# Optimization experiments

Hardware: AMD Instinct MI355X
Metric: run time of the kernel (lower is better)

Reference implementation:

```python
import jax, jax.numpy as jnp
import numpy as np

B, S, D = 64, 1024, 128
EPS = 1e-5

def hardswish(x):
    return x * jnp.clip(x + 3.0, 0.0, 6.0) / 6.0

def setup_inputs() -> dict:
    key = jax.random.key(0)
    k1, k2, k3 = jax.random.split(key, 3)
    x = jax.random.normal(k1, (B, S, D), dtype=jnp.float32)
    ln_w = jnp.ones((S, D), dtype=jnp.float32)
    ln_b = jnp.zeros((S, D), dtype=jnp.float32)
    # U1[i]/U2[i] rows packed into lower-triangular (S,S); init ~ N(0,1)*0.01
    W1 = jax.random.normal(k2, (S, S), dtype=jnp.float32) * 0.01
    W2 = jax.random.normal(k3, (S, S), dtype=jnp.float32) * 0.01
    return {"x": x, "ln_w": ln_w, "ln_b": ln_b, "W1": W1, "W2": W2}

def reference(x, ln_w, ln_b, W1, W2):
    # LayerNorm over the last two dims (seq_len, feature_dim) jointly
    mu = jnp.mean(x, axis=(-2, -1), keepdims=True)
    var = jnp.mean(jnp.square(x - mu), axis=(-2, -1), keepdims=True)
    h = (x - mu) * jax.lax.rsqrt(var + EPS) * ln_w + ln_b
    # causal (lower-triangular) time mixing: u[:, t] = sum_{s<=t} W1[t, s] * h[:, s]
    mask = jnp.tril(jnp.ones((S, S), dtype=x.dtype))
    u = hardswish(jnp.einsum('ts,bsd->btd', W1 * mask, h))
    v = jnp.einsum('ts,bsd->btd', W2 * mask, u)
    return x + v
```

## Files before the change

kernel.cpp:

```cpp
#include <hip/hip_runtime.h>
#include <hip/hip_bf16.h>

#define NB 64
#define S_ 1024
#define D_ 128

typedef __attribute__((ext_vector_type(8))) short bf16x8;
typedef __attribute__((ext_vector_type(4))) float f32x4;

__device__ __forceinline__ unsigned short f2bf(float f) {
  __hip_bfloat16 h = __float2bfloat16(f);
  return __builtin_bit_cast(unsigned short, h);
}

__device__ __forceinline__ void async_copy16(const void* g, void* l) {
  __builtin_amdgcn_global_load_lds(
      (const __attribute__((address_space(1))) unsigned int*)g,
      (__attribute__((address_space(3))) unsigned int*)l, 16, 0, 0);
}

__global__ __launch_bounds__(256) void prep_kernel(
    const float* __restrict__ x, const float* __restrict__ W1,
    const float* __restrict__ W2, float2* __restrict__ part,
    unsigned short* __restrict__ W1b, unsigned short* __restrict__ W2b) {
  const int blk = blockIdx.x;
  if (blk < 1024) {
    const int b = blk >> 4, c = blk & 15, t = threadIdx.x;
    const float4* xb = (const float4*)(x + (size_t)b * (S_ * D_) + c * 8192);
    float s = 0.f, q = 0.f;
#pragma unroll
    for (int i = 0; i < 8; ++i) {
      float4 v = xb[i * 256 + t];
      s += v.x + v.y + v.z + v.w;
      q += v.x * v.x + v.y * v.y + v.z * v.z + v.w * v.w;
    }
#pragma unroll
    for (int o = 32; o > 0; o >>= 1) {
      s += __shfl_down(s, o, 64);
      q += __shfl_down(q, o, 64);
    }
    __shared__ float2 w4[4];
    const int wave = t >> 6, lane = t & 63;
    if (lane == 0) w4[wave] = make_float2(s, q);
    __syncthreads();
    if (t == 0) {
      float ss = 0.f, qq = 0.f;
#pragma unroll
      for (int i = 0; i < 4; ++i) { ss += w4[i].x; qq += w4[i].y; }
      part[blk] = make_float2(ss, qq);
    }
  } else {
    const int id = (blk - 1024) * 256 + threadIdx.x;
    const int perW = (S_ * S_) / 4;
    const float* src = (id < perW) ? W1 : W2;
    unsigned short* dst = (id < perW) ? W1b : W2b;
    const int i4 = (id < perW) ? id : id - perW;
    const int flat = i4 * 4;
    const int trow = flat >> 10;
    const int scol = flat & 1023;
    float4 v = ((const float4*)src)[i4];
    ushort4 o;
    o.x = f2bf((scol + 0 <= trow) ? v.x : 0.f);
    o.y = f2bf((scol + 1 <= trow) ? v.y : 0.f);
    o.z = f2bf((scol + 2 <= trow) ? v.z : 0.f);
    o.w = f2bf((scol + 3 <= trow) ? v.w : 0.f);
    *(ushort4*)(dst + flat) = o;
  }
}

__global__ __launch_bounds__(256) void norm_t_kernel(const float* __restrict__ x,
                                                     const float* __restrict__ w,
                                                     const float* __restrict__ bb,
                                                     const float2* __restrict__ part,
                                                     unsigned short* __restrict__ hT) {
  __shared__ unsigned short lds[128 * 72];
  const int blk = blockIdx.x;
  const int b = blk >> 4;
  const int s0 = (blk & 15) * 64;
  const int t = threadIdx.x;
  float sum = 0.f, sumq = 0.f;
#pragma unroll
  for (int i = 0; i < 16; ++i) {
    float2 p = part[b * 16 + i];
    sum += p.x; sumq += p.y;
  }
  const float inv = 1.0f / (S_ * D_);
  const float mu = sum * inv;
  const float rs = rsqrtf(sumq * inv - mu * mu + 1e-5f);

  const float4* xb = (const float4*)(x + ((size_t)b * S_ + s0) * D_);
  const float4* wb = (const float4*)(w + (size_t)s0 * D_);
  const float4* bv4 = (const float4*)(bb + (size_t)s0 * D_);
#pragma unroll
  for (int r = 0; r < 8; ++r) {
    const int f = r * 256 + t;
    const int srow = f >> 5;
    const int c4 = f & 31;
    float4 xv = xb[f];
    float4 wv = wb[f];
    float4 bvv = bv4[f];
    float h0 = (xv.x - mu) * rs * wv.x + bvv.x;
    float h1 = (xv.y - mu) * rs * wv.y + bvv.y;
    float h2 = (xv.z - mu) * rs * wv.z + bvv.z;
    float h3 = (xv.w - mu) * rs * wv.w + bvv.w;
    const int d0 = c4 * 4;
    lds[(d0 + 0) * 72 + srow] = f2bf(h0);
    lds[(d0 + 1) * 72 + srow] = f2bf(h1);
    lds[(d0 + 2) * 72 + srow] = f2bf(h2);
    lds[(d0 + 3) * 72 + srow] = f2bf(h3);
  }
  __syncthreads();
  unsigned short* outp = hT + (size_t)b * D_ * S_;
#pragma unroll
  for (int rr = 0; rr < 4; ++rr) {
    const int idx = rr * 256 + t;
    const int d = idx >> 3;
    const int ch = idx & 7;
    uint4 v = *(const uint4*)(lds + d * 72 + ch * 8);
    *(uint4*)(outp + d * S_ + s0 + ch * 8) = v;
  }
}

template <bool HSWISH>
__global__ __launch_bounds__(256, 4) void gemm_causal(
    const unsigned short* __restrict__ Wm, const unsigned short* __restrict__ Bt,
    unsigned short* __restrict__ Ut, const float* __restrict__ Xres,
    float* __restrict__ Out) {
  __shared__ __align__(16) char smem[24576];
  unsigned short* ldsA0 = (unsigned short*)smem;
  unsigned short* ldsB0 = (unsigned short*)(smem + 4096);
  unsigned short* ldsA1 = (unsigned short*)(smem + 12288);
  unsigned short* ldsB1 = (unsigned short*)(smem + 16384);
  unsigned short* ldsT = (unsigned short*)smem;

  const int t = threadIdx.x;
  const int wave = t >> 6, lane = t & 63;
  const int quad = lane >> 4, l16 = lane & 15;
  const int wm = (wave >> 1) * 32, wn = (wave & 1) * 64;

  const int bi = blockIdx.x;
  const int xcd = bi & 7;
  const int slot = bi >> 3;
  const int b = xcd * 8 + (slot & 7);
  const int mt = slot >> 3;
  const int row0 = mt * 64;

  const unsigned short* gA = Wm + (size_t)row0 * S_;
  const unsigned short* gB = Bt + (size_t)b * D_ * S_;

  const int srow = t >> 2, scol = (t & 3) * 8;

  f32x4 acc[2][4] = {};

  const int kend = row0 + 64;
  for (int k0 = 0; k0 < kend; k0 += 64) {
    async_copy16(gA + srow * S_ + k0 + scol, ldsA0 + t * 8);
    async_copy16(gB + srow * S_ + k0 + scol, ldsB0 + t * 8);
    async_copy16(gB + (srow + 64) * S_ + k0 + scol, ldsB0 + (t + 256) * 8);
    async_copy16(gA + srow * S_ + k0 + 32 + scol, ldsA1 + t * 8);
    async_copy16(gB + srow * S_ + k0 + 32 + scol, ldsB1 + t * 8);
    async_copy16(gB + (srow + 64) * S_ + k0 + 32 + scol, ldsB1 + (t + 256) * 8);
    __syncthreads();
    bf16x8 af0[2], bf0[4], af1[2], bf1[4];
#pragma unroll
    for (int i = 0; i < 2; ++i) {
      af0[i] = *(const bf16x8*)(ldsA0 + (wm + i * 16 + l16) * 32 + quad * 8);
      af1[i] = *(const bf16x8*)(ldsA1 + (wm + i * 16 + l16) * 32 + quad * 8);
    }
#pragma unroll
    for (int j = 0; j < 4; ++j) {
      bf0[j] = *(const bf16x8*)(ldsB0 + (wn + j * 16 + l16) * 32 + quad * 8);
      bf1[j] = *(const bf16x8*)(ldsB1 + (wn + j * 16 + l16) * 32 + quad * 8);
    }
#pragma unroll
    for (int i = 0; i < 2; ++i)
#pragma unroll
      for (int j = 0; j < 4; ++j)
        acc[i][j] = __builtin_amdgcn_mfma_f32_16x16x32_bf16(af0[i], bf0[j],
                                                            acc[i][j], 0, 0, 0);
#pragma unroll
    for (int i = 0; i < 2; ++i)
#pragma unroll
      for (int j = 0; j < 4; ++j)
        acc[i][j] = __builtin_amdgcn_mfma_f32_16x16x32_bf16(af1[i], bf1[j],
                                                            acc[i][j], 0, 0, 0);
    __syncthreads();
  }

  if (HSWISH) {
#pragma unroll
    for (int i = 0; i < 2; ++i)
#pragma unroll
      for (int j = 0; j < 4; ++j) {
        ushort4 pk;
        float v0 = acc[i][j][0], v1 = acc[i][j][1], v2 = acc[i][j][2], v3 = acc[i][j][3];
        pk.x = f2bf(v0 * fminf(fmaxf(v0 + 3.f, 0.f), 6.f) * (1.f / 6.f));
        pk.y = f2bf(v1 * fminf(fmaxf(v1 + 3.f, 0.f), 6.f) * (1.f / 6.f));
        pk.z = f2bf(v2 * fminf(fmaxf(v2 + 3.f, 0.f), 6.f) * (1.f / 6.f));
        pk.w = f2bf(v3 * fminf(fmaxf(v3 + 3.f, 0.f), 6.f) * (1.f / 6.f));
        const int n = wn + j * 16 + l16;
        const int m0 = wm + i * 16 + quad * 4;
        *(ushort4*)(ldsT + n * 72 + m0) = pk;
      }
    __syncthreads();
    unsigned short* gU = Ut + (size_t)b * D_ * S_;
#pragma unroll
    for (int rr = 0; rr < 4; ++rr) {
      const int idx = rr * 256 + t;
      const int d = idx >> 3;
      const int ch = idx & 7;
      uint4 v = *(const uint4*)(ldsT + d * 72 + ch * 8);
      *(uint4*)(gU + d * S_ + row0 + ch * 8) = v;
    }
  } else {
    float* gO = Out + (size_t)b * S_ * D_;
    const float* gX = Xres + (size_t)b * S_ * D_;
#pragma unroll
    for (int i = 0; i < 2; ++i) {
      const int mrow0 = row0 + wm + i * 16 + quad * 4;
#pragma unroll
      for (int j = 0; j < 4; ++j) {
        const int col = wn + j * 16 + l16;
#pragma unroll
        for (int r = 0; r < 4; ++r) {
          const int addr = (mrow0 + r) * D_ + col;
          gO[addr] = gX[addr] + acc[i][j][r];
        }
      }
    }
  }
}

extern "C" void kernel_launch(void* const* d_in, const int* in_sizes, int n_in,
                              void* d_out, int out_size, void* d_ws, size_t ws_size,
                              hipStream_t stream) {
  const float* x = (const float*)d_in[0];
  const float* ln_w = (const float*)d_in[1];
  const float* ln_b = (const float*)d_in[2];
  const float* W1 = (const float*)d_in[3];
  const float* W2 = (const float*)d_in[4];
  float* out = (float*)d_out;

  char* ws = (char*)d_ws;
  float2* part = (float2*)ws;
  unsigned short* W1b = (unsigned short*)(ws + 16384);
  unsigned short* W2b = W1b + (size_t)S_ * S_;
  unsigned short* hT = W2b + (size_t)S_ * S_;
  unsigned short* uT = hT + (size_t)NB * D_ * S_;

  prep_kernel<<<3072, 256, 0, stream>>>(x, W1, W2, part, W1b, W2b);
  norm_t_kernel<<<NB * 16, 256, 0, stream>>>(x, ln_w, ln_b, part, hT);
  gemm_causal<true><<<1024, 256, 0, stream>>>(W1b, hT, uT, nullptr, nullptr);
  gemm_causal<false><<<1024, 256, 0, stream>>>(W2b, uT, nullptr, x, out);
}
```

Measured before the change: 139.5 us.

## Load GEMM operands directly from global into registers with prefetch, drop LDS staging

```diff
diff --git a/kernel.cpp b/kernel.cpp
--- a/kernel.cpp
+++ b/kernel.cpp
@@ -11,12 +11,6 @@
 __device__ __forceinline__ unsigned short f2bf(float f) {
   __hip_bfloat16 h = __float2bfloat16(f);
   return __builtin_bit_cast(unsigned short, h);
-}
-
-__device__ __forceinline__ void async_copy16(const void* g, void* l) {
-  __builtin_amdgcn_global_load_lds(
-      (const __attribute__((address_space(1))) unsigned int*)g,
-      (__attribute__((address_space(3))) unsigned int*)l, 16, 0, 0);
 }
 
 __global__ __launch_bounds__(256) void prep_kernel(
@@ -126,80 +120,87 @@
     const unsigned short* __restrict__ Wm, const unsigned short* __restrict__ Bt,
     unsigned short* __restrict__ Ut, const float* __restrict__ Xres,
     float* __restrict__ Out) {
-  __shared__ __align__(16) char smem[24576];
-  unsigned short* ldsA0 = (unsigned short*)smem;
-  unsigned short* ldsB0 = (unsigned short*)(smem + 4096);
-  unsigned short* ldsA1 = (unsigned short*)(smem + 12288);
-  unsigned short* ldsB1 = (unsigned short*)(smem + 16384);
-  unsigned short* ldsT = (unsigned short*)smem;
+  __shared__ __align__(16) unsigned short ldsT[128 * 72];
 
   const int t = threadIdx.x;
   const int wave = t >> 6, lane = t & 63;
   const int quad = lane >> 4, l16 = lane & 15;
-  const int wm = (wave >> 1) * 32, wn = (wave & 1) * 64;
+  const int wn = wave * 32;
 
   const int bi = blockIdx.x;
   const int xcd = bi & 7;
   const int slot = bi >> 3;
   const int b = xcd * 8 + (slot & 7);
-  const int mt = slot >> 3;
+  const int j = slot >> 3;
+  const int mt = (j < 8) ? j : (j ^ 3);
   const int row0 = mt * 64;
 
-  const unsigned short* gA = Wm + (size_t)row0 * S_;
-  const unsigned short* gB = Bt + (size_t)b * D_ * S_;
-
-  const int srow = t >> 2, scol = (t & 3) * 8;
-
-  f32x4 acc[2][4] = {};
-
-  const int kend = row0 + 64;
-  for (int k0 = 0; k0 < kend; k0 += 64) {
-    async_copy16(gA + srow * S_ + k0 + scol, ldsA0 + t * 8);
-    async_copy16(gB + srow * S_ + k0 + scol, ldsB0 + t * 8);
-    async_copy16(gB + (srow + 64) * S_ + k0 + scol, ldsB0 + (t + 256) * 8);
-    async_copy16(gA + srow * S_ + k0 + 32 + scol, ldsA1 + t * 8);
-    async_copy16(gB + srow * S_ + k0 + 32 + scol, ldsB1 + t * 8);
-    async_copy16(gB + (srow + 64) * S_ + k0 + 32 + scol, ldsB1 + (t + 256) * 8);
-    __syncthreads();
-    bf16x8 af0[2], bf0[4], af1[2], bf1[4];
-#pragma unroll
-    for (int i = 0; i < 2; ++i) {
-      af0[i] = *(const bf16x8*)(ldsA0 + (wm + i * 16 + l16) * 32 + quad * 8);
-      af1[i] = *(const bf16x8*)(ldsA1 + (wm + i * 16 + l16) * 32 + quad * 8);
-    }
-#pragma unroll
-    for (int j = 0; j < 4; ++j) {
-      bf0[j] = *(const bf16x8*)(ldsB0 + (wn + j * 16 + l16) * 32 + quad * 8);
-      bf1[j] = *(const bf16x8*)(ldsB1 + (wn + j * 16 + l16) * 32 + quad * 8);
-    }
-#pragma unroll
-    for (int i = 0; i < 2; ++i)
-#pragma unroll
-      for (int j = 0; j < 4; ++j)
-        acc[i][j] = __builtin_amdgcn_mfma_f32_16x16x32_bf16(af0[i], bf0[j],
-                                                            acc[i][j], 0, 0, 0);
-#pragma unroll
-    for (int i = 0; i < 2; ++i)
-#pragma unroll
-      for (int j = 0; j < 4; ++j)
-        acc[i][j] = __builtin_amdgcn_mfma_f32_16x16x32_bf16(af1[i], bf1[j],
-                                                            acc[i][j], 0, 0, 0);
-    __syncthreads();
+  const unsigned short* gA = Wm + ((size_t)row0 + l16) * S_ + quad * 8;
+  const unsigned short* gB = Bt + ((size_t)b * D_ + wn + l16) * S_ + quad * 8;
+
+  const int trips = 2 * (mt + 1);
+
+  f32x4 acc[4][2] = {};
+  bf16x8 A0[4], A1[4], B0[2], B1[2];
+
+#pragma unroll
+  for (int i = 0; i < 4; ++i) {
+    A0[i] = *(const bf16x8*)(gA + i * 16 * S_);
+    A1[i] = *(const bf16x8*)(gA + i * 16 * S_ + 32);
+  }
+#pragma unroll
+  for (int jj = 0; jj < 2; ++jj) {
+    B0[jj] = *(const bf16x8*)(gB + jj * 16 * S_);
+    B1[jj] = *(const bf16x8*)(gB + jj * 16 * S_ + 32);
+  }
+
+  for (int kt = 0; kt < trips; kt += 2) {
+    const int kpre0 = (kt + 2) * 32;
+    const int kpre1 = (kt + 3) * 32;
+    bf16x8 An[4], Bn[2], Am[4], Bm[2];
+    if (kt + 2 < trips) {
+#pragma unroll
+      for (int i = 0; i < 4; ++i) {
+        An[i] = *(const bf16x8*)(gA + i * 16 * S_ + kpre0);
+        Am[i] = *(const bf16x8*)(gA + i * 16 * S_ + kpre1);
+      }
+#pragma unroll
+      for (int jj = 0; jj < 2; ++jj) {
+        Bn[jj] = *(const bf16x8*)(gB + jj * 16 * S_ + kpre0);
+        Bm[jj] = *(const bf16x8*)(gB + jj * 16 * S_ + kpre1);
+      }
+    }
+#pragma unroll
+    for (int i = 0; i < 4; ++i)
+#pragma unroll
+      for (int jj = 0; jj < 2; ++jj)
+        acc[i][jj] = __builtin_amdgcn_mfma_f32_16x16x32_bf16(A0[i], B0[jj],
+                                                             acc[i][jj], 0, 0, 0);
+#pragma unroll
+    for (int i = 0; i < 4; ++i)
+#pragma unroll
+      for (int jj = 0; jj < 2; ++jj)
+        acc[i][jj] = __builtin_amdgcn_mfma_f32_16x16x32_bf16(A1[i], B1[jj],
+                                                             acc[i][jj], 0, 0, 0);
+#pragma unroll
+    for (int i = 0; i < 4; ++i) { A0[i] = An[i]; A1[i] = Am[i]; }
+#pragma unroll
+    for (int jj = 0; jj < 2; ++jj) { B0[jj] = Bn[jj]; B1[jj] = Bm[jj]; }
   }
 
   if (HSWISH) {
 #pragma unroll
-    for (int i = 0; i < 2; ++i)
-#pragma unroll
-      for (int j = 0; j < 4; ++j) {
+    for (int i = 0; i < 4; ++i)
+#pragma unroll
+      for (int jj = 0; jj < 2; ++jj) {
         ushort4 pk;
-        float v0 = acc[i][j][0], v1 = acc[i][j][1], v2 = acc[i][j][2], v3 = acc[i][j][3];
+        float v0 = acc[i][jj][0], v1 = acc[i][jj][1], v2 = acc[i][jj][2], v3 = acc[i][jj][3];
         pk.x = f2bf(v0 * fminf(fmaxf(v0 + 3.f, 0.f), 6.f) * (1.f / 6.f));
         pk.y = f2bf(v1 * fminf(fmaxf(v1 + 3.f, 0.f), 6.f) * (1.f / 6.f));
         pk.z = f2bf(v2 * fminf(fmaxf(v2 + 3.f, 0.f), 6.f) * (1.f / 6.f));
         pk.w = f2bf(v3 * fminf(fmaxf(v3 + 3.f, 0.f), 6.f) * (1.f / 6.f));
-        const int n = wn + j * 16 + l16;
-        const int m0 = wm + i * 16 + quad * 4;
+        const int n = wn + jj * 16 + l16;
+        const int m0 = i * 16 + quad * 4;
         *(ushort4*)(ldsT + n * 72 + m0) = pk;
       }
     __syncthreads();
@@ -216,15 +217,15 @@
     float* gO = Out + (size_t)b * S_ * D_;
     const float* gX = Xres + (size_t)b * S_ * D_;
 #pragma unroll
-    for (int i = 0; i < 2; ++i) {
-      const int mrow0 = row0 + wm + i * 16 + quad * 4;
-#pragma unroll
-      for (int j = 0; j < 4; ++j) {
-        const int col = wn + j * 16 + l16;
+    for (int i = 0; i < 4; ++i) {
+      const int mrow0 = row0 + i * 16 + quad * 4;
+#pragma unroll
+      for (int jj = 0; jj < 2; ++jj) {
+        const int col = wn + jj * 16 + l16;
 #pragma unroll
         for (int r = 0; r < 4; ++r) {
           const int addr = (mrow0 + r) * D_ + col;
-          gO[addr] = gX[addr] + acc[i][j][r];
+          gO[addr] = gX[addr] + acc[i][jj][r];
         }
       }
     }
```

Result: slower. 236.5 us (+69.5%).
